# Optimization experiments

Hardware: AMD Instinct MI355X
Metric: run time of the kernel (lower is better)

The kernel has to match this reference:

```python
import jax, jax.numpy as jnp
import numpy as np

N, E, F_IN, HID, K, CLS = 50000, 800000, 512, 128, 4, 40
EPS = 0.3


def setup_inputs() -> dict:
    key = jax.random.key(0)
    ks = jax.random.split(key, 6)
    x = jax.random.normal(ks[0], (N, F_IN), dtype=jnp.float32)
    edge_index = jax.random.randint(ks[1], (2, E), 0, N, dtype=jnp.int32)
    # xavier_normal with gain=1.414 ~ gain*sqrt(2/(fan_in+fan_out))
    t1_w = jax.random.normal(ks[2], (HID, F_IN), jnp.float32) * (1.414 * np.sqrt(2.0 / (F_IN + HID)))
    t1_b = jnp.zeros((HID,), jnp.float32)
    gate_w = jax.random.normal(ks[3], (K, 2 * HID), jnp.float32) * (1.414 * np.sqrt(2.0 / (2 * HID + 1)))
    gate_b = jnp.zeros((K,), jnp.float32)
    t2_w = jax.random.normal(ks[4], (CLS, HID), jnp.float32) * (1.414 * np.sqrt(2.0 / (HID + CLS)))
    t2_b = jnp.zeros((CLS,), jnp.float32)
    return dict(x=x, edge_index=edge_index, t1_w=t1_w, t1_b=t1_b,
                gate_w=gate_w, gate_b=gate_b, t2_w=t2_w, t2_b=t2_b)


def _fa_layer(h, row, col, nd, gw, gb):
    # gate(cat[h_row, h_col]) as two matvecs (equivalent to concat + Linear)
    d = h.shape[1]
    g = jnp.tanh(h[row] @ gw[:d] + h[col] @ gw[d:] + gb)   # [E]
    norm = g * nd[row] * nd[col]                           # [E]
    msg = norm[:, None] * h[row]                           # x_j = h[source], [E, HID]
    # aggregate (add) into target nodes
    return jax.ops.segment_sum(msg, col, num_segments=h.shape[0])


def reference(x, edge_index, t1_w, t1_b, gate_w, gate_b, t2_w, t2_b):
    row, col = edge_index[0], edge_index[1]
    deg = jax.ops.segment_sum(jnp.ones((E,), x.dtype), row, num_segments=N)
    nd = jnp.clip(deg, 1.0, None) ** -0.5                  # degree^{-1/2}, clamped at 1
    h = jax.nn.relu(x @ t1_w.T + t1_b)                     # [N, HID]
    raw = h
    for k in range(K):
        h = EPS * raw + _fa_layer(h, row, col, nd, gate_w[k], gate_b[k])
    return jax.nn.log_softmax(h @ t2_w.T + t2_b, axis=1)   # [N, CLS]
```

## Files before the change

### kernel.cpp

```cpp
#include <hip/hip_runtime.h>
#include <math.h>

#define N_NODES 50000
#define N_EDGES 800000
#define F_IN    512
#define HID     128
#define K_LAYERS 4
#define N_CLS   40
#define EPS_C   0.3f
#define CAP     64

typedef __bf16 bf16x8 __attribute__((ext_vector_type(8)));
typedef float  f32x4  __attribute__((ext_vector_type(4)));

__device__ inline unsigned short bfb(float f) {
    __bf16 b = (__bf16)f;
    return __builtin_bit_cast(unsigned short, b);
}
__device__ inline unsigned pack2(float a, float b) {
    return (unsigned)bfb(a) | ((unsigned)bfb(b) << 16);
}
__device__ inline float lo2(unsigned v) { return __builtin_bit_cast(float, v << 16); }
__device__ inline float hi2(unsigned v) { return __builtin_bit_cast(float, v & 0xffff0000u); }
__device__ inline bf16x8 ld_frag(const unsigned short* p) {
    uint4 q = *(const uint4*)p;
    return __builtin_bit_cast(bf16x8, q);
}

__global__ void k_nd(const int* __restrict__ deg, float* __restrict__ nd) {
    int i = blockIdx.x * blockDim.x + threadIdx.x;
    if (i < N_NODES) {
        float d = fmaxf((float)deg[i], 1.0f);
        nd[i] = 1.0f / sqrtf(d);
    }
}

#define GS 72
#define EPB 2048
__global__ __launch_bounds__(256) void k_gemm_mfma(const float* __restrict__ x,
                                                   const float* __restrict__ w,
                                                   const float* __restrict__ bias,
                                                   float* __restrict__ h0,
                                                   const int* __restrict__ row,
                                                   const int* __restrict__ col,
                                                   int* __restrict__ deg,
                                                   int* __restrict__ cur,
                                                   int* __restrict__ bucket) {
    {
        int e0 = blockIdx.x * EPB + threadIdx.x;
#pragma unroll
        for (int q = 0; q < EPB / 256; q++) {
            int e = e0 + q * 256;
            if (e < N_EDGES) {
                int r = row[e], c = col[e];
                atomicAdd(&deg[r], 1);
                int p = atomicAdd(&cur[c], 1);
                if (p < CAP) bucket[((size_t)c << 6) + p] = r;
            }
        }
    }

    __shared__ __attribute__((aligned(16))) unsigned short As[128 * GS];
    __shared__ __attribute__((aligned(16))) unsigned short Bs[128 * GS];
    const int t    = threadIdx.x;
    const int lane = t & 63;
    const int wv   = t >> 6;
    const int wrow = wv >> 1;
    const int wcol = wv & 1;
    const int nb0  = blockIdx.x * 128;
    const int m16  = lane & 15;
    const int quad = lane >> 4;

    f32x4 acc[4][4];
#pragma unroll
    for (int mi = 0; mi < 4; mi++)
#pragma unroll
        for (int ni = 0; ni < 4; ni++) acc[mi][ni] = (f32x4){0.f, 0.f, 0.f, 0.f};

    for (int k0 = 0; k0 < F_IN; k0 += 64) {
        __syncthreads();
        {
            int r  = t & 127;
            int kh = (t >> 7) * 32;
            int n  = nb0 + r;
            unsigned short* pl = &As[r * GS + kh];
            if (n < N_NODES) {
                const float* px = &x[(size_t)n * F_IN + k0 + kh];
#pragma unroll
                for (int q = 0; q < 4; q++) {
                    float4 f0 = *(const float4*)(px + q * 8);
                    float4 f1 = *(const float4*)(px + q * 8 + 4);
                    *(ushort4*)(pl + q * 8)     = make_ushort4(bfb(f0.x), bfb(f0.y), bfb(f0.z), bfb(f0.w));
                    *(ushort4*)(pl + q * 8 + 4) = make_ushort4(bfb(f1.x), bfb(f1.y), bfb(f1.z), bfb(f1.w));
                }
            } else {
#pragma unroll
                for (int q = 0; q < 8; q++) *(ushort4*)(pl + q * 4) = make_ushort4(0, 0, 0, 0);
            }
        }
        {
            int j  = t & 127;
            int kh = (t >> 7) * 32;
            const float* pw = &w[(size_t)j * F_IN + k0 + kh];
            unsigned short* pl = &Bs[j * GS + kh];
#pragma unroll
            for (int q = 0; q < 4; q++) {
                float4 f0 = *(const float4*)(pw + q * 8);
                float4 f1 = *(const float4*)(pw + q * 8 + 4);
                *(ushort4*)(pl + q * 8)     = make_ushort4(bfb(f0.x), bfb(f0.y), bfb(f0.z), bfb(f0.w));
                *(ushort4*)(pl + q * 8 + 4) = make_ushort4(bfb(f1.x), bfb(f1.y), bfb(f1.z), bfb(f1.w));
            }
        }
        __syncthreads();
#pragma unroll
        for (int kk = 0; kk < 64; kk += 32) {
            bf16x8 af[4], bfr[4];
#pragma unroll
            for (int mi = 0; mi < 4; mi++)
                af[mi] = ld_frag(&As[(wrow * 64 + mi * 16 + m16) * GS + kk + quad * 8]);
#pragma unroll
            for (int ni = 0; ni < 4; ni++)
                bfr[ni] = ld_frag(&Bs[(wcol * 64 + ni * 16 + m16) * GS + kk + quad * 8]);
#pragma unroll
            for (int mi = 0; mi < 4; mi++)
#pragma unroll
                for (int ni = 0; ni < 4; ni++)
                    acc[mi][ni] = __builtin_amdgcn_mfma_f32_16x16x32_bf16(af[mi], bfr[ni], acc[mi][ni], 0, 0, 0);
        }
    }
    float bj[4];
#pragma unroll
    for (int ni = 0; ni < 4; ni++) bj[ni] = bias[wcol * 64 + ni * 16 + m16];
#pragma unroll
    for (int mi = 0; mi < 4; mi++)
#pragma unroll
        for (int reg = 0; reg < 4; reg++) {
            int n = nb0 + wrow * 64 + mi * 16 + quad * 4 + reg;
            if (n < N_NODES) {
#pragma unroll
                for (int ni = 0; ni < 4; ni++)
                    h0[(size_t)n * HID + wcol * 64 + ni * 16 + m16] =
                        fmaxf(acc[mi][ni][reg] + bj[ni], 0.f);
            }
        }
}

__global__ __launch_bounds__(256) void k_h2b_ab(const float* __restrict__ raw,
                                                const float* __restrict__ nd,
                                                const float* __restrict__ gw,
                                                unsigned* __restrict__ h0b,
                                                float2* __restrict__ pn0,
                                                float* __restrict__ bn0) {
    const int node = blockIdx.x * 4 + (threadIdx.x >> 6);
    const int lane = threadIdx.x & 63;
    if (node >= N_NODES) return;
    float2 hv = ((const float2*)raw)[((size_t)node << 6) + lane];
    h0b[((size_t)node << 6) + lane] = pack2(hv.x, hv.y);
    float pa = hv.x * gw[2 * lane]       + hv.y * gw[2 * lane + 1];
    float pb = hv.x * gw[128 + 2 * lane] + hv.y * gw[129 + 2 * lane];
#pragma unroll
    for (int d = 32; d > 0; d >>= 1) {
        pa += __shfl_xor(pa, d);
        pb += __shfl_xor(pb, d);
    }
    if (lane == 0) { pn0[node] = make_float2(pa, nd[node]); bn0[node] = pb; }
}

__global__ __launch_bounds__(256) void k_agg6(const unsigned* __restrict__ hb,
                                              const float* __restrict__ raw,
                                              const float2* __restrict__ pn,
                                              const float* __restrict__ bn,
                                              const int* __restrict__ bucket,
                                              const int* __restrict__ cur,
                                              const float* __restrict__ gb_all, int k,
                                              unsigned* __restrict__ outb,
                                              const float* __restrict__ gwn,
                                              float2* __restrict__ pnn,
                                              float* __restrict__ bnn) {
    const int node = blockIdx.x * 4 + (threadIdx.x >> 6);
    const int lane = threadIdx.x & 63;
    if (node >= N_NODES) return;
    const int esub = lane >> 4;
    const int fg   = lane & 15;
    const int cnt  = min(cur[node], CAP);
    const float ndc = pn[node].y;
    const float bw  = bn[node] + gb_all[k];

    int   idx = 0;
    float g   = 0.f;
    if (lane < cnt) {
        idx = bucket[((size_t)node << 6) + lane];
        float2 pr = pn[idx];
        g = tanhf(pr.x + bw) * pr.y * ndc;
    }

    float acc[8];
#pragma unroll
    for (int j = 0; j < 8; j++) acc[j] = 0.f;

    const uint4* hb4 = (const uint4*)hb;
    for (int base = 0; base < cnt; base += 8) {
        int p0 = base + esub;
        int p1 = p0 + 4;
        int   e0 = __shfl(idx, p0);
        int   e1 = __shfl(idx, p1);
        float g0 = __shfl(g, p0);
        float g1 = __shfl(g, p1);
        uint4 v0 = hb4[(size_t)e0 * 16 + fg];
        uint4 v1 = hb4[(size_t)e1 * 16 + fg];
        acc[0] = fmaf(g0, lo2(v0.x), acc[0]); acc[1] = fmaf(g0, hi2(v0.x), acc[1]);
        acc[2] = fmaf(g0, lo2(v0.y), acc[2]); acc[3] = fmaf(g0, hi2(v0.y), acc[3]);
        acc[4] = fmaf(g0, lo2(v0.z), acc[4]); acc[5] = fmaf(g0, hi2(v0.z), acc[5]);
        acc[6] = fmaf(g0, lo2(v0.w), acc[6]); acc[7] = fmaf(g0, hi2(v0.w), acc[7]);
        acc[0] = fmaf(g1, lo2(v1.x), acc[0]); acc[1] = fmaf(g1, hi2(v1.x), acc[1]);
        acc[2] = fmaf(g1, lo2(v1.y), acc[2]); acc[3] = fmaf(g1, hi2(v1.y), acc[3]);
        acc[4] = fmaf(g1, lo2(v1.z), acc[4]); acc[5] = fmaf(g1, hi2(v1.z), acc[5]);
        acc[6] = fmaf(g1, lo2(v1.w), acc[6]); acc[7] = fmaf(g1, hi2(v1.w), acc[7]);
    }

#pragma unroll
    for (int j = 0; j < 8; j++) {
        acc[j] += __shfl_xor(acc[j], 16);
        acc[j] += __shfl_xor(acc[j], 32);
    }

    const float4* raw4 = (const float4*)raw;
    float4 r0 = raw4[(size_t)node * 32 + 2 * fg];
    float4 r1 = raw4[(size_t)node * 32 + 2 * fg + 1];
    float of[8];
    of[0] = fmaf(EPS_C, r0.x, acc[0]); of[1] = fmaf(EPS_C, r0.y, acc[1]);
    of[2] = fmaf(EPS_C, r0.z, acc[2]); of[3] = fmaf(EPS_C, r0.w, acc[3]);
    of[4] = fmaf(EPS_C, r1.x, acc[4]); of[5] = fmaf(EPS_C, r1.y, acc[5]);
    of[6] = fmaf(EPS_C, r1.z, acc[6]); of[7] = fmaf(EPS_C, r1.w, acc[7]);
    if (esub == 0) {
        uint4 ov;
        ov.x = pack2(of[0], of[1]); ov.y = pack2(of[2], of[3]);
        ov.z = pack2(of[4], of[5]); ov.w = pack2(of[6], of[7]);
        ((uint4*)outb)[(size_t)node * 16 + fg] = ov;
    }

    if (gwn) {
        const float4* gw4 = (const float4*)gwn;
        float4 wa0 = gw4[fg * 2], wa1 = gw4[fg * 2 + 1];
        float4 wb0 = gw4[32 + fg * 2], wb1 = gw4[32 + fg * 2 + 1];
        float pa = of[0] * wa0.x + of[1] * wa0.y + of[2] * wa0.z + of[3] * wa0.w
                 + of[4] * wa1.x + of[5] * wa1.y + of[6] * wa1.z + of[7] * wa1.w;
        float pb = of[0] * wb0.x + of[1] * wb0.y + of[2] * wb0.z + of[3] * wb0.w
                 + of[4] * wb1.x + of[5] * wb1.y + of[6] * wb1.z + of[7] * wb1.w;
#pragma unroll
        for (int d = 1; d <= 8; d <<= 1) {
            pa += __shfl_xor(pa, d);
            pb += __shfl_xor(pb, d);
        }
        if (lane == 0) { pnn[node] = make_float2(pa, ndc); bnn[node] = pb; }
    }
}

__global__ __launch_bounds__(256) void k_out(const unsigned* __restrict__ hb,
                                             const float* __restrict__ w2,
                                             const float* __restrict__ b2,
                                             float* __restrict__ out) {
    __shared__ float ws[N_CLS][HID + 1];
    __shared__ float hs[4][HID];
    __shared__ float bs[N_CLS];
    const int t = threadIdx.x;
    for (int i = t; i < N_CLS * HID; i += 256) {
        ws[i / HID][i % HID] = w2[i];
    }
    if (t < N_CLS) bs[t] = b2[t];
    int wv = t >> 6, lane = t & 63;
    int node = blockIdx.x * 4 + wv;
    if (node < N_NODES) {
        unsigned v = hb[((size_t)node << 6) + lane];
        hs[wv][2 * lane]     = lo2(v);
        hs[wv][2 * lane + 1] = hi2(v);
    }
    __syncthreads();
    float z = -INFINITY;
    if (node < N_NODES && lane < N_CLS) {
        float s = bs[lane];
#pragma unroll 8
        for (int kk = 0; kk < HID; kk++) s = fmaf(hs[wv][kk], ws[lane][kk], s);
        z = s;
    }
    float mx = z;
#pragma unroll
    for (int d = 32; d > 0; d >>= 1) mx = fmaxf(mx, __shfl_xor(mx, d));
    float ex = (z == -INFINITY) ? 0.f : expf(z - mx);
    float sum = ex;
#pragma unroll
    for (int d = 32; d > 0; d >>= 1) sum += __shfl_xor(sum, d);
    if (node < N_NODES && lane < N_CLS)
        out[(size_t)node * N_CLS + lane] = z - mx - logf(sum);
}

extern "C" void kernel_launch(void* const* d_in, const int* in_sizes, int n_in,
                              void* d_out, int out_size, void* d_ws, size_t ws_size,
                              hipStream_t stream) {
    const float* x   = (const float*)d_in[0];
    const int*   ei  = (const int*)d_in[1];
    const float* t1w = (const float*)d_in[2];
    const float* t1b = (const float*)d_in[3];
    const float* gw  = (const float*)d_in[4];
    const float* gb  = (const float*)d_in[5];
    const float* t2w = (const float*)d_in[6];
    const float* t2b = (const float*)d_in[7];
    float* out = (float*)d_out;

    const int* row = ei;
    const int* col = ei + N_EDGES;

    char* p = (char*)d_ws;
    auto alloc = [&](size_t bytes) -> char* {
        char* q = p;
        p += (bytes + 255) & ~(size_t)255;
        return q;
    };
    float*    raw    = (float*)alloc(sizeof(float) * (size_t)N_NODES * HID);
    unsigned* h0b    = (unsigned*)alloc(sizeof(unsigned) * (size_t)N_NODES * 64);
    unsigned* hA     = (unsigned*)alloc(sizeof(unsigned) * (size_t)N_NODES * 64);
    unsigned* hB     = (unsigned*)alloc(sizeof(unsigned) * (size_t)N_NODES * 64);
    float2*   pn0    = (float2*)alloc(sizeof(float2) * N_NODES);
    float2*   pn1    = (float2*)alloc(sizeof(float2) * N_NODES);
    float*    bn0    = (float*)alloc(sizeof(float) * N_NODES);
    float*    bn1    = (float*)alloc(sizeof(float) * N_NODES);
    float*    nd     = (float*)alloc(sizeof(float) * N_NODES);
    int*      degi   = (int*)alloc(sizeof(int) * N_NODES);
    int*      cur    = (int*)alloc(sizeof(int) * N_NODES);
    int*      bucket = (int*)alloc(sizeof(int) * (size_t)N_NODES * CAP);

    hipMemsetAsync(degi, 0, sizeof(int) * N_NODES, stream);
    hipMemsetAsync(cur,  0, sizeof(int) * N_NODES, stream);

    const int nb = (N_NODES + 255) / 256;
    const int wb = (N_NODES + 3) / 4;
    const int gb_blocks = (N_NODES + 127) / 128;

    k_gemm_mfma<<<gb_blocks, 256, 0, stream>>>(x, t1w, t1b, raw,
                                               row, col, degi, cur, bucket);
    k_nd<<<nb, 256, 0, stream>>>(degi, nd);
    k_h2b_ab<<<wb, 256, 0, stream>>>(raw, nd, gw, h0b, pn0, bn0);

    const unsigned* hc = h0b;
    unsigned* ring[2] = {hA, hB};
    const float2* pc = pn0;  float2* pnx = pn1;
    const float*  bc = bn0;  float*  bnx = bn1;
    for (int k = 0; k < K_LAYERS; k++) {
        unsigned* hn = ring[k & 1];
        const float* gwn = (k + 1 < K_LAYERS) ? (gw + (size_t)(k + 1) * 2 * HID) : nullptr;
        k_agg6<<<wb, 256, 0, stream>>>(hc, raw, pc, bc, bucket, cur, gb, k, hn, gwn, pnx, bnx);
        hc = hn;
        const float2* tp = pc; pc = pnx; pnx = (float2*)tp;
        const float*  tb = bc; bc = bnx; bnx = (float*)tb;
    }

    k_out<<<wb, 256, 0, stream>>>(hc, t2w, t2b, out);
}
```

Measured before the change: 457.3 us.

## Split edge bucketing into dedicated blocks, fold nd into prep, unroll gather

Edge bucketing, which each GEMM block used to run as a prologue over 2048 edges, now runs in 3125 separate blocks of the same launch that handle one edge per thread and then exit. GEMM tiles no longer wait on atomics before starting. The separate degree-normalisation kernel is removed and its rsqrt is computed inside k_h2b_ab, saving a launch and a buffer round trip. The aggregation loop now issues four neighbour gathers per iteration instead of two, for more memory-level parallelism at the cost of extra registers and wasted loads on low-degree nodes.

New measurement: 417.1 us. -8.8%, faster.

```diff
diff --git a/kernel.cpp b/kernel.cpp
--- a/kernel.cpp
+++ b/kernel.cpp
@@ -10,6 +10,9 @@
 #define EPS_C   0.3f
 #define CAP     64
 
+#define GB_BLOCKS 391
+#define PB_BLOCKS 3125
+
 typedef __bf16 bf16x8 __attribute__((ext_vector_type(8)));
 typedef float  f32x4  __attribute__((ext_vector_type(4)));
 
@@ -27,17 +30,8 @@
     return __builtin_bit_cast(bf16x8, q);
 }
 
-__global__ void k_nd(const int* __restrict__ deg, float* __restrict__ nd) {
-    int i = blockIdx.x * blockDim.x + threadIdx.x;
-    if (i < N_NODES) {
-        float d = fmaxf((float)deg[i], 1.0f);
-        nd[i] = 1.0f / sqrtf(d);
-    }
-}
-
 #define GS 72
-#define EPB 2048
-__global__ __launch_bounds__(256) void k_gemm_mfma(const float* __restrict__ x,
+__global__ __launch_bounds__(256) void k_gemm_prep(const float* __restrict__ x,
                                                    const float* __restrict__ w,
                                                    const float* __restrict__ bias,
                                                    float* __restrict__ h0,
@@ -46,18 +40,15 @@
                                                    int* __restrict__ deg,
                                                    int* __restrict__ cur,
                                                    int* __restrict__ bucket) {
-    {
-        int e0 = blockIdx.x * EPB + threadIdx.x;
-#pragma unroll
-        for (int q = 0; q < EPB / 256; q++) {
-            int e = e0 + q * 256;
-            if (e < N_EDGES) {
-                int r = row[e], c = col[e];
-                atomicAdd(&deg[r], 1);
-                int p = atomicAdd(&cur[c], 1);
-                if (p < CAP) bucket[((size_t)c << 6) + p] = r;
-            }
-        }
+    if (blockIdx.x >= GB_BLOCKS) {
+        int e = (blockIdx.x - GB_BLOCKS) * 256 + threadIdx.x;
+        if (e < N_EDGES) {
+            int r = row[e], c = col[e];
+            atomicAdd(&deg[r], 1);
+            int p = atomicAdd(&cur[c], 1);
+            if (p < CAP) bucket[((size_t)c << 6) + p] = r;
+        }
+        return;
     }
 
     __shared__ __attribute__((aligned(16))) unsigned short As[128 * GS];
@@ -146,7 +137,7 @@
 }
 
 __global__ __launch_bounds__(256) void k_h2b_ab(const float* __restrict__ raw,
-                                                const float* __restrict__ nd,
+                                                const int* __restrict__ deg,
                                                 const float* __restrict__ gw,
                                                 unsigned* __restrict__ h0b,
                                                 float2* __restrict__ pn0,
@@ -163,7 +154,11 @@
         pa += __shfl_xor(pa, d);
         pb += __shfl_xor(pb, d);
     }
-    if (lane == 0) { pn0[node] = make_float2(pa, nd[node]); bn0[node] = pb; }
+    if (lane == 0) {
+        float dv = fmaxf((float)deg[node], 1.0f);
+        pn0[node] = make_float2(pa, 1.0f / sqrtf(dv));
+        bn0[node] = pb;
+    }
 }
 
 __global__ __launch_bounds__(256) void k_agg6(const unsigned* __restrict__ hb,
@@ -199,15 +194,17 @@
     for (int j = 0; j < 8; j++) acc[j] = 0.f;
 
     const uint4* hb4 = (const uint4*)hb;
-    for (int base = 0; base < cnt; base += 8) {
+    for (int base = 0; base < cnt; base += 16) {
         int p0 = base + esub;
-        int p1 = p0 + 4;
-        int   e0 = __shfl(idx, p0);
-        int   e1 = __shfl(idx, p1);
-        float g0 = __shfl(g, p0);
-        float g1 = __shfl(g, p1);
+        int p1 = p0 + 4, p2 = p0 + 8, p3 = p0 + 12;
+        int   e0 = __shfl(idx, p0), e1 = __shfl(idx, p1);
+        int   e2 = __shfl(idx, p2), e3 = __shfl(idx, p3);
+        float g0 = __shfl(g, p0),   g1 = __shfl(g, p1);
+        float g2 = __shfl(g, p2),   g3 = __shfl(g, p3);
         uint4 v0 = hb4[(size_t)e0 * 16 + fg];
         uint4 v1 = hb4[(size_t)e1 * 16 + fg];
+        uint4 v2 = hb4[(size_t)e2 * 16 + fg];
+        uint4 v3 = hb4[(size_t)e3 * 16 + fg];
         acc[0] = fmaf(g0, lo2(v0.x), acc[0]); acc[1] = fmaf(g0, hi2(v0.x), acc[1]);
         acc[2] = fmaf(g0, lo2(v0.y), acc[2]); acc[3] = fmaf(g0, hi2(v0.y), acc[3]);
         acc[4] = fmaf(g0, lo2(v0.z), acc[4]); acc[5] = fmaf(g0, hi2(v0.z), acc[5]);
@@ -216,6 +213,14 @@
         acc[2] = fmaf(g1, lo2(v1.y), acc[2]); acc[3] = fmaf(g1, hi2(v1.y), acc[3]);
         acc[4] = fmaf(g1, lo2(v1.z), acc[4]); acc[5] = fmaf(g1, hi2(v1.z), acc[5]);
         acc[6] = fmaf(g1, lo2(v1.w), acc[6]); acc[7] = fmaf(g1, hi2(v1.w), acc[7]);
+        acc[0] = fmaf(g2, lo2(v2.x), acc[0]); acc[1] = fmaf(g2, hi2(v2.x), acc[1]);
+        acc[2] = fmaf(g2, lo2(v2.y), acc[2]); acc[3] = fmaf(g2, hi2(v2.y), acc[3]);
+        acc[4] = fmaf(g2, lo2(v2.z), acc[4]); acc[5] = fmaf(g2, hi2(v2.z), acc[5]);
+        acc[6] = fmaf(g2, lo2(v2.w), acc[6]); acc[7] = fmaf(g2, hi2(v2.w), acc[7]);
+        acc[0] = fmaf(g3, lo2(v3.x), acc[0]); acc[1] = fmaf(g3, hi2(v3.x), acc[1]);
+        acc[2] = fmaf(g3, lo2(v3.y), acc[2]); acc[3] = fmaf(g3, hi2(v3.y), acc[3]);
+        acc[4] = fmaf(g3, lo2(v3.z), acc[4]); acc[5] = fmaf(g3, hi2(v3.z), acc[5]);
+        acc[6] = fmaf(g3, lo2(v3.w), acc[6]); acc[7] = fmaf(g3, hi2(v3.w), acc[7]);
     }
 
 #pragma unroll
@@ -324,7 +329,6 @@
     float2*   pn1    = (float2*)alloc(sizeof(float2) * N_NODES);
     float*    bn0    = (float*)alloc(sizeof(float) * N_NODES);
     float*    bn1    = (float*)alloc(sizeof(float) * N_NODES);
-    float*    nd     = (float*)alloc(sizeof(float) * N_NODES);
     int*      degi   = (int*)alloc(sizeof(int) * N_NODES);
     int*      cur    = (int*)alloc(sizeof(int) * N_NODES);
     int*      bucket = (int*)alloc(sizeof(int) * (size_t)N_NODES * CAP);
@@ -332,14 +336,11 @@
     hipMemsetAsync(degi, 0, sizeof(int) * N_NODES, stream);
     hipMemsetAsync(cur,  0, sizeof(int) * N_NODES, stream);
 
-    const int nb = (N_NODES + 255) / 256;
     const int wb = (N_NODES + 3) / 4;
-    const int gb_blocks = (N_NODES + 127) / 128;
-
-    k_gemm_mfma<<<gb_blocks, 256, 0, stream>>>(x, t1w, t1b, raw,
-                                               row, col, degi, cur, bucket);
-    k_nd<<<nb, 256, 0, stream>>>(degi, nd);
-    k_h2b_ab<<<wb, 256, 0, stream>>>(raw, nd, gw, h0b, pn0, bn0);
+
+    k_gemm_prep<<<GB_BLOCKS + PB_BLOCKS, 256, 0, stream>>>(x, t1w, t1b, raw,
+                                                           row, col, degi, cur, bucket);
+    k_h2b_ab<<<wb, 256, 0, stream>>>(raw, degi, gw, h0b, pn0, bn0);
 
     const unsigned* hc = h0b;
     unsigned* ring[2] = {hA, hB};
```
